# Performance work log

Measured on AMD Instinct MI355X. Metric: run time of the kernel, lower is better.

Reference implementation:

```python
import math
import jax, jax.numpy as jnp
import numpy as np

N = 8192
IN_DIM = 512
INTER = 512
HID = 1024
OUT = 512
GROUPS = 16
EPS = 1e-5


def setup_inputs() -> dict:
    key = jax.random.key(0)
    ks = jax.random.split(key, 12)
    w = lambda k, shape: jax.random.normal(k, shape, jnp.float32) * 0.02
    return {
        "h": jax.random.normal(ks[0], (N, IN_DIM), jnp.float32),
        "D": jax.random.uniform(ks[1], (N, N), dtype=jnp.float32),
        "h_prime": jax.random.normal(ks[2], (N, OUT), jnp.float32),
        "Wq": w(ks[3], (INTER, IN_DIM)), "bq": jnp.zeros((INTER,), jnp.float32),
        "Wk": w(ks[4], (INTER, IN_DIM)), "bk": jnp.zeros((INTER,), jnp.float32),
        "Wv": w(ks[5], (INTER, IN_DIM)), "bv": jnp.zeros((INTER,), jnp.float32),
        "Wr": w(ks[6], (HID, INTER)), "br": jnp.zeros((HID,), jnp.float32),
        "Wc": w(ks[7], (HID, OUT)), "bc": jnp.zeros((HID,), jnp.float32),
        "Wp": w(ks[8], (OUT, 2 * HID)), "bp": jnp.zeros((OUT,), jnp.float32),
        "alpha": jnp.full((OUT,), 0.25, jnp.float32),       # PReLU per-channel slope
        "gamma": jnp.ones((OUT,), jnp.float32),             # GroupNorm weight
        "beta": jnp.zeros((OUT,), jnp.float32),             # GroupNorm bias
    }


def reference(h, D, h_prime, Wq, bq, Wk, bk, Wv, bv, Wr, br, Wc, bc, Wp, bp, alpha, gamma, beta):
    Q = h @ Wq.T + bq                                    # [N, inter]
    K = h @ Wk.T + bk
    V = h @ Wv.T + bv
    scores = (Q @ K.T) / math.sqrt(INTER)                # [N, N]
    attn = jax.nn.softmax(D * scores, axis=-1)           # decay-masked softmax
    h_ret = attn @ V                                     # [N, inter]
    h_ret = jax.nn.gelu(h_ret @ Wr.T + br, approximate=False)  # torch GELU (erf)
    h_cat = h_prime @ Wc.T + bc                          # [N, hid]
    x = jnp.concatenate([h_ret, h_cat], axis=-1) @ Wp.T + bp   # [N, out]
    x = jnp.where(x >= 0, x, alpha * x)                  # PReLU, per-channel
    # GroupNorm over [1, out, N]: stats per group over (channels_in_group, N)
    xT = x.T                                             # [out, N]
    grp = xT.reshape(GROUPS, (OUT // GROUPS) * N)
    mean = grp.mean(axis=1, keepdims=True)
    var = grp.var(axis=1, keepdims=True)
    grp = (grp - mean) * jax.lax.rsqrt(var + EPS)
    xT = grp.reshape(OUT, N) * gamma[:, None] + beta[:, None]
    return xT.T                                          # [N, out]
```

## Files before the change

### kernel.cpp

```cpp
#include <hip/hip_runtime.h>
#include <stdint.h>
#include <math.h>

typedef float f32x4 __attribute__((ext_vector_type(4)));
typedef __bf16 bf16x8 __attribute__((ext_vector_type(8)));
typedef unsigned short u16;

#define DEVINL static __device__ __forceinline__

DEVINL u16 f2bf(float f) {
  union { float f; unsigned u; } x; x.f = f;
  unsigned r = x.u + 0x7fffu + ((x.u >> 16) & 1u);
  return (u16)(r >> 16);
}

DEVINL void gload_lds16(const void* g, void* l) {
  __builtin_amdgcn_global_load_lds(
      (__attribute__((address_space(1))) void*)(g),
      (__attribute__((address_space(3))) void*)(l), 16, 0, 0);
}

__global__ void cast_kernel(const float* __restrict__ src, u16* __restrict__ dst, int n) {
  int i = (blockIdx.x * 256 + threadIdx.x) * 4;
  if (i >= n) return;
  float4 v = *(const float4*)(src + i);
  u16 o[4] = { f2bf(v.x), f2bf(v.y), f2bf(v.z), f2bf(v.w) };
  *(uint64_t*)(dst + i) = *(uint64_t*)o;
}

template<int EPI>
__global__ __launch_bounds__(256, 2) void gemm_nt(
    const u16* __restrict__ A, int lda, const u16* __restrict__ B, int ldb,
    void* __restrict__ C, int ldc, int coff,
    const float* __restrict__ bias, const float* __restrict__ alpha,
    int N128, int K, float scale)
{
  __shared__ __align__(16) u16 at[2][128 * 64];
  __shared__ __align__(16) u16 bt[2][128 * 64];
  const int tid = threadIdx.x;
  const int w = tid >> 6, lane = tid & 63, r = lane & 15, kg = lane >> 4;
  const int bm = blockIdx.x / N128, bn = blockIdx.x % N128;
  const int m0 = bm * 128, n0 = bn * 128;

  f32x4 acc[4][4];
  #pragma unroll
  for (int m = 0; m < 4; ++m)
    #pragma unroll
    for (int n = 0; n < 4; ++n) acc[m][n] = f32x4{0.f, 0.f, 0.f, 0.f};

  const int srow = tid >> 3, sc = tid & 7;
  const int nk = K >> 6;

  #pragma unroll
  for (int i = 0; i < 4; ++i) {
    int row = srow + i * 32, cs = (sc ^ row) & 7;
    gload_lds16(A + (size_t)(m0 + row) * lda + cs * 8, at[0] + i * 2048 + w * 512);
    gload_lds16(B + (size_t)(n0 + row) * ldb + cs * 8, bt[0] + i * 2048 + w * 512);
  }
  __syncthreads();

  for (int kt = 0; kt < nk; ++kt) {
    const int cur = kt & 1;
    if (kt + 1 < nk) {
      #pragma unroll
      for (int i = 0; i < 4; ++i) {
        int row = srow + i * 32, cs = (sc ^ row) & 7;
        int kcol = (kt + 1) * 64 + cs * 8;
        gload_lds16(A + (size_t)(m0 + row) * lda + kcol, at[cur ^ 1] + i * 2048 + w * 512);
        gload_lds16(B + (size_t)(n0 + row) * ldb + kcol, bt[cur ^ 1] + i * 2048 + w * 512);
      }
    }
    #pragma unroll
    for (int ks = 0; ks < 2; ++ks) {
      bf16x8 af[4], bff[4];
      #pragma unroll
      for (int m = 0; m < 4; ++m) {
        int row = (w >> 1) * 64 + m * 16 + r;
        int cs = ((ks * 4 + kg) ^ row) & 7;
        af[m] = *(const bf16x8*)(at[cur] + row * 64 + cs * 8);
      }
      #pragma unroll
      for (int n = 0; n < 4; ++n) {
        int row = (w & 1) * 64 + n * 16 + r;
        int cs = ((ks * 4 + kg) ^ row) & 7;
        bff[n] = *(const bf16x8*)(bt[cur] + row * 64 + cs * 8);
      }
      #pragma unroll
      for (int m = 0; m < 4; ++m)
        #pragma unroll
        for (int n = 0; n < 4; ++n)
          acc[m][n] = __builtin_amdgcn_mfma_f32_16x16x32_bf16(af[m], bff[n], acc[m][n], 0, 0, 0);
    }
    __syncthreads();
  }

  #pragma unroll
  for (int m = 0; m < 4; ++m) {
    #pragma unroll
    for (int n = 0; n < 4; ++n) {
      const int gcol = n0 + (w & 1) * 64 + n * 16 + r;
      #pragma unroll
      for (int reg = 0; reg < 4; ++reg) {
        const int grow = m0 + (w >> 1) * 64 + m * 16 + kg * 4 + reg;
        float v = acc[m][n][reg];
        if (EPI == 1) v += bias[grow]; else v += bias[gcol];
        if (EPI == 0) v *= scale;
        if (EPI == 2) v = 0.5f * v * (1.f + erff(v * 0.70710678118654752f));
        if (EPI == 3) {
          float a = alpha[gcol];
          v = (v >= 0.f) ? v : a * v;
          ((float*)C)[(size_t)grow * ldc + coff + gcol] = v;
        } else {
          ((u16*)C)[(size_t)grow * ldc + coff + gcol] = f2bf(v);
        }
      }
    }
  }
}

__global__ __launch_bounds__(256, 2) void flash_kernel(
    const u16* __restrict__ Qb, const u16* __restrict__ Kb,
    const u16* __restrict__ VTb, const float* __restrict__ Dm,
    float* __restrict__ Op, float* __restrict__ lp)
{
  __shared__ __align__(16) u16 kbuf[2][64 * 128];
  __shared__ __align__(16) u16 vbuf[2][128 * 64];
  __shared__ __align__(16) u16 pbuf[4][16 * 64];
  const int tid = threadIdx.x;
  const int w = tid >> 6, lane = tid & 63, r = lane & 15, kg = lane >> 4;
  const int s = blockIdx.x & 3, qb = blockIdx.x >> 2;
  const int q0 = qb * 64;
  const int kvb = s * 2048;

  auto stage_k = [&](int buf, int kv0, int kc) {
    #pragma unroll
    for (int i = 0; i < 4; ++i) {
      const int row = (tid >> 4) + i * 16, c = tid & 15;
      const int cs = (c & 8) | ((c ^ row) & 7);
      gload_lds16(Kb + (size_t)(kv0 + row) * 512 + kc * 128 + cs * 8,
                  kbuf[buf] + i * 2048 + w * 512);
    }
  };
  auto stage_v = [&](int buf, int kv0, int dc) {
    #pragma unroll
    for (int i = 0; i < 4; ++i) {
      const int row = (tid >> 3) + i * 32, c = tid & 7;
      const int cs = (c ^ row) & 7;
      gload_lds16(VTb + (size_t)(dc * 128 + row) * 8192 + kv0 + cs * 8,
                  vbuf[buf] + i * 2048 + w * 512);
    }
  };

  bf16x8 aq[16];
  {
    const u16* qrow = Qb + (size_t)(q0 + w * 16 + r) * 512;
    #pragma unroll
    for (int ks = 0; ks < 16; ++ks) aq[ks] = *(const bf16x8*)(qrow + ks * 32 + kg * 8);
  }

  f32x4 o[32];
  #pragma unroll
  for (int i = 0; i < 32; ++i) o[i] = f32x4{0.f, 0.f, 0.f, 0.f};
  float lsum[4] = {0.f, 0.f, 0.f, 0.f};

  stage_k(0, kvb, 0);
  __syncthreads();

  #pragma unroll 1
  for (int j = 0; j < 32; ++j) {
    const int kv0 = kvb + j * 64;
    f32x4 sacc[4];
    #pragma unroll
    for (int t = 0; t < 4; ++t) sacc[t] = f32x4{0.f, 0.f, 0.f, 0.f};
    float dv[4][4];

    #pragma unroll
    for (int kc = 0; kc < 4; ++kc) {
      if (kc < 3) stage_k((kc + 1) & 1, kv0, kc + 1);
      else        stage_v(0, kv0, 0);
      if (kc == 1) {
        const float* db = Dm + (size_t)(q0 + w * 16 + kg * 4) * 8192 + kv0 + r;
        #pragma unroll
        for (int t = 0; t < 4; ++t)
          #pragma unroll
          for (int reg = 0; reg < 4; ++reg)
            dv[t][reg] = __builtin_nontemporal_load(db + (size_t)reg * 8192 + t * 16);
      }
      #pragma unroll
      for (int ks2 = 0; ks2 < 4; ++ks2) {
        const bf16x8 a = aq[kc * 4 + ks2];
        #pragma unroll
        for (int t = 0; t < 4; ++t) {
          const int row = t * 16 + r;
          const int c = ks2 * 4 + kg;
          const int cs = (c & 8) | ((c ^ row) & 7);
          const bf16x8 b = *(const bf16x8*)(kbuf[kc & 1] + row * 128 + cs * 8);
          sacc[t] = __builtin_amdgcn_mfma_f32_16x16x32_bf16(a, b, sacc[t], 0, 0, 0);
        }
      }
      if (kc == 3) {
        #pragma unroll
        for (int t = 0; t < 4; ++t) {
          #pragma unroll
          for (int reg = 0; reg < 4; ++reg) {
            const float pv = __expf(sacc[t][reg] * dv[t][reg]);
            lsum[reg] += pv;
            const int prow = kg * 4 + reg, pcol = t * 16 + r;
            const int byt = prow * 128 + (((pcol >> 3) ^ prow) & 7) * 16 + (pcol & 7) * 2;
            *(u16*)((char*)pbuf[w] + byt) = f2bf(pv);
          }
        }
      }
      __syncthreads();
    }

    bf16x8 ap[2];
    #pragma unroll
    for (int ks = 0; ks < 2; ++ks) {
      const int cs = ((ks * 4 + kg) ^ r) & 7;
      ap[ks] = *(const bf16x8*)((const char*)pbuf[w] + r * 128 + cs * 16);
    }

    #pragma unroll
    for (int dc = 0; dc < 4; ++dc) {
      if (dc < 3)        stage_v((dc + 1) & 1, kv0, dc + 1);
      else if (j < 31)   stage_k(0, kv0 + 64, 0);
      #pragma unroll
      for (int t2 = 0; t2 < 8; ++t2) {
        const int row = t2 * 16 + r;
        #pragma unroll
        for (int ks = 0; ks < 2; ++ks) {
          const int cs = ((ks * 4 + kg) ^ row) & 7;
          const bf16x8 b = *(const bf16x8*)(vbuf[dc & 1] + row * 64 + cs * 8);
          o[dc * 8 + t2] = __builtin_amdgcn_mfma_f32_16x16x32_bf16(ap[ks], b, o[dc * 8 + t2], 0, 0, 0);
        }
      }
      __syncthreads();
    }
  }

  #pragma unroll
  for (int reg = 0; reg < 4; ++reg) {
    float v = lsum[reg];
    v += __shfl_xor(v, 1); v += __shfl_xor(v, 2);
    v += __shfl_xor(v, 4); v += __shfl_xor(v, 8);
    lsum[reg] = v;
  }

  float* ob = Op + (size_t)s * (8192 * 512) + (size_t)(q0 + w * 16 + kg * 4) * 512 + r;
  #pragma unroll
  for (int ti = 0; ti < 32; ++ti)
    #pragma unroll
    for (int reg = 0; reg < 4; ++reg)
      ob[(size_t)reg * 512 + ti * 16] = o[ti][reg];

  if (r == 0) {
    #pragma unroll
    for (int reg = 0; reg < 4; ++reg)
      lp[(size_t)s * 8192 + q0 + w * 16 + kg * 4 + reg] = lsum[reg];
  }
}

__global__ void combine_kernel(const float* __restrict__ Op, const float* __restrict__ lp,
                               u16* __restrict__ hrb) {
  const int idx = (blockIdx.x * 256 + threadIdx.x) * 4;
  const int q = idx >> 9;
  const float li = 1.f / (lp[q] + lp[8192 + q] + lp[16384 + q] + lp[24576 + q]);
  float4 a = *(const float4*)(Op + idx);
  const float4 b = *(const float4*)(Op + 4194304 + idx);
  const float4 c = *(const float4*)(Op + 8388608 + idx);
  const float4 d = *(const float4*)(Op + 12582912 + idx);
  a.x += b.x + c.x + d.x; a.y += b.y + c.y + d.y;
  a.z += b.z + c.z + d.z; a.w += b.w + c.w + d.w;
  u16 o[4] = { f2bf(a.x * li), f2bf(a.y * li), f2bf(a.z * li), f2bf(a.w * li) };
  *(uint64_t*)(hrb + idx) = *(uint64_t*)o;
}

__global__ void gn_stats_kernel(const float* __restrict__ x, float* __restrict__ part) {
  const int g = blockIdx.x >> 4, ch = blockIdx.x & 15;
  const int t = threadIdx.x;
  float s = 0.f, ss = 0.f;
  const int cl = (t & 7) * 4;
  const int r0 = ch * 512 + (t >> 3);
  for (int i = 0; i < 16; ++i) {
    const float4 v = *(const float4*)(x + (size_t)(r0 + i * 32) * 512 + g * 32 + cl);
    s += v.x + v.y + v.z + v.w;
    ss += v.x * v.x + v.y * v.y + v.z * v.z + v.w * v.w;
  }
  #pragma unroll
  for (int m = 1; m < 64; m <<= 1) { s += __shfl_xor(s, m); ss += __shfl_xor(ss, m); }
  __shared__ float red[8];
  const int w = t >> 6, lane = t & 63;
  if (lane == 0) { red[w * 2] = s; red[w * 2 + 1] = ss; }
  __syncthreads();
  if (t == 0) {
    part[blockIdx.x * 2]     = red[0] + red[2] + red[4] + red[6];
    part[blockIdx.x * 2 + 1] = red[1] + red[3] + red[5] + red[7];
  }
}

__global__ void gn_finalize_kernel(const float* __restrict__ part, float* __restrict__ mv) {
  const int g = threadIdx.x;
  if (g < 16) {
    float s = 0.f, ss = 0.f;
    for (int ch = 0; ch < 16; ++ch) {
      s  += part[(g * 16 + ch) * 2];
      ss += part[(g * 16 + ch) * 2 + 1];
    }
    const float mean = s * (1.f / 262144.f);
    const float var = ss * (1.f / 262144.f) - mean * mean;
    mv[g * 2] = mean;
    mv[g * 2 + 1] = rsqrtf(var + 1e-5f);
  }
}

__global__ void gn_norm_kernel(const float* __restrict__ x, const float* __restrict__ mv,
                               const float* __restrict__ gamma, const float* __restrict__ beta,
                               float* __restrict__ out) {
  const int idx = (blockIdx.x * 256 + threadIdx.x) * 4;
  const int c = idx & 511, g = c >> 5;
  const float mean = mv[g * 2], rs = mv[g * 2 + 1];
  float4 v = *(const float4*)(x + idx);
  const float4 gm = *(const float4*)(gamma + c);
  const float4 bt = *(const float4*)(beta + c);
  v.x = (v.x - mean) * rs * gm.x + bt.x;
  v.y = (v.y - mean) * rs * gm.y + bt.y;
  v.z = (v.z - mean) * rs * gm.z + bt.z;
  v.w = (v.w - mean) * rs * gm.w + bt.w;
  *(float4*)(out + idx) = v;
}

extern "C" void kernel_launch(void* const* d_in, const int* in_sizes, int n_in,
                              void* d_out, int out_size, void* d_ws, size_t ws_size,
                              hipStream_t stream) {
  (void)in_sizes; (void)n_in; (void)out_size; (void)ws_size;
  const float* h     = (const float*)d_in[0];
  const float* Dm    = (const float*)d_in[1];
  const float* hp    = (const float*)d_in[2];
  const float* Wq    = (const float*)d_in[3];
  const float* bq    = (const float*)d_in[4];
  const float* Wk    = (const float*)d_in[5];
  const float* bk    = (const float*)d_in[6];
  const float* Wv    = (const float*)d_in[7];
  const float* bv    = (const float*)d_in[8];
  const float* Wr    = (const float*)d_in[9];
  const float* br    = (const float*)d_in[10];
  const float* Wc    = (const float*)d_in[11];
  const float* bc    = (const float*)d_in[12];
  const float* Wp    = (const float*)d_in[13];
  const float* bp    = (const float*)d_in[14];
  const float* alpha = (const float*)d_in[15];
  const float* gamma = (const float*)d_in[16];
  const float* beta  = (const float*)d_in[17];

  char* ws = (char*)d_ws;
  u16*   hb   = (u16*)(ws + 0);
  u16*   hpb  = (u16*)(ws + 8388608);
  u16*   Qb   = (u16*)(ws + 16777216);
  u16*   Kb   = (u16*)(ws + 25165824);
  u16*   VTb  = (u16*)(ws + 33554432);
  u16*   hrb  = (u16*)(ws + 41943040);
  u16*   Wqb  = (u16*)(ws + 50331648);
  u16*   Wkb  = (u16*)(ws + 50855936);
  u16*   Wvb  = (u16*)(ws + 51380224);
  u16*   Wrb  = (u16*)(ws + 51904512);
  u16*   Wcb  = (u16*)(ws + 52953088);
  u16*   Wpb  = (u16*)(ws + 54001664);
  u16*   xcat = (u16*)(ws + 56098816);
  float* xf   = (float*)(ws + 89653248);
  float* Op   = (float*)(ws + 106430464);
  float* lp   = (float*)(ws + 173539328);
  float* gp   = (float*)(ws + 173670400);
  float* mv   = (float*)(ws + 173672448);

  cast_kernel<<<4096, 256, 0, stream>>>(h, hb, 4194304);
  cast_kernel<<<4096, 256, 0, stream>>>(hp, hpb, 4194304);
  cast_kernel<<<256, 256, 0, stream>>>(Wq, Wqb, 262144);
  cast_kernel<<<256, 256, 0, stream>>>(Wk, Wkb, 262144);
  cast_kernel<<<256, 256, 0, stream>>>(Wv, Wvb, 262144);
  cast_kernel<<<512, 256, 0, stream>>>(Wr, Wrb, 524288);
  cast_kernel<<<512, 256, 0, stream>>>(Wc, Wcb, 524288);
  cast_kernel<<<1024, 256, 0, stream>>>(Wp, Wpb, 1048576);

  gemm_nt<0><<<256, 256, 0, stream>>>(hb, 512, Wqb, 512, Qb, 512, 0, bq, nullptr, 4, 512, 0.044194173824159216f);
  gemm_nt<0><<<256, 256, 0, stream>>>(hb, 512, Wkb, 512, Kb, 512, 0, bk, nullptr, 4, 512, 1.0f);
  gemm_nt<1><<<256, 256, 0, stream>>>(Wvb, 512, hb, 512, VTb, 8192, 0, bv, nullptr, 64, 512, 1.0f);

  flash_kernel<<<512, 256, 0, stream>>>(Qb, Kb, VTb, Dm, Op, lp);
  combine_kernel<<<4096, 256, 0, stream>>>(Op, lp, hrb);

  gemm_nt<2><<<512, 256, 0, stream>>>(hrb, 512, Wrb, 512, xcat, 2048, 0, br, nullptr, 8, 512, 1.0f);
  gemm_nt<0><<<512, 256, 0, stream>>>(hpb, 512, Wcb, 512, xcat, 2048, 1024, bc, nullptr, 8, 512, 1.0f);
  gemm_nt<3><<<256, 256, 0, stream>>>(xcat, 2048, Wpb, 2048, xf, 512, 0, bp, alpha, 4, 2048, 1.0f);

  gn_stats_kernel<<<256, 256, 0, stream>>>(xf, gp);
  gn_finalize_kernel<<<1, 64, 0, stream>>>(gp, mv);
  gn_norm_kernel<<<4096, 256, 0, stream>>>(xf, mv, gamma, beta, (float*)d_out);
}
```

Before: 504.1 us.

## Replace K/V double buffers with a 4-slot LDS ring prefetched three stages ahead

The flash kernel's separate K and V double buffers become a single 4-slot LDS ring fed by a 9-phase schedule per KV tile: 4 K chunks, 1 D tile, then 4 V chunks. Loads are issued three phases ahead and gated by s_waitcnt vmcnt plus one barrier per phase, instead of the old synchronous refill pattern. The decay matrix D is now staged through LDS with async global-to-LDS loads rather than read directly into registers, and the MFMA sections are wrapped in s_setprio raises. This aims to hide global memory latency better and reduce barrier stalls, at the cost of more complex ring indexing and a redundant prefetch on the last iteration.

```diff
diff --git a/kernel.cpp b/kernel.cpp
--- a/kernel.cpp
+++ b/kernel.cpp
@@ -123,8 +123,7 @@
     const u16* __restrict__ VTb, const float* __restrict__ Dm,
     float* __restrict__ Op, float* __restrict__ lp)
 {
-  __shared__ __align__(16) u16 kbuf[2][64 * 128];
-  __shared__ __align__(16) u16 vbuf[2][128 * 64];
+  __shared__ __align__(16) u16 ring[4][8192];
   __shared__ __align__(16) u16 pbuf[4][16 * 64];
   const int tid = threadIdx.x;
   const int w = tid >> 6, lane = tid & 63, r = lane & 15, kg = lane >> 4;
@@ -132,22 +131,37 @@
   const int q0 = qb * 64;
   const int kvb = s * 2048;
 
-  auto stage_k = [&](int buf, int kv0, int kc) {
+  const int rK = tid >> 4, cK = tid & 15;
+  const int rV = tid >> 3, cV = tid & 7;
+
+  auto issueK = [&](int jj, int kc, int buf) {
+    const u16* src = Kb + (size_t)(kvb + jj * 64) * 512 + kc * 128;
+    u16* dst = ring[buf];
     #pragma unroll
     for (int i = 0; i < 4; ++i) {
-      const int row = (tid >> 4) + i * 16, c = tid & 15;
-      const int cs = (c & 8) | ((c ^ row) & 7);
-      gload_lds16(Kb + (size_t)(kv0 + row) * 512 + kc * 128 + cs * 8,
-                  kbuf[buf] + i * 2048 + w * 512);
+      const int row = rK + i * 16;
+      const int cs = (cK & 8) | ((cK ^ row) & 7);
+      gload_lds16(src + (size_t)row * 512 + cs * 8, dst + i * 2048 + w * 512);
     }
   };
-  auto stage_v = [&](int buf, int kv0, int dc) {
+  auto issueD = [&](int jj, int buf) {
+    const float* src = Dm + (size_t)q0 * 8192 + kvb + jj * 64;
+    u16* dst = ring[buf];
     #pragma unroll
     for (int i = 0; i < 4; ++i) {
-      const int row = (tid >> 3) + i * 32, c = tid & 7;
-      const int cs = (c ^ row) & 7;
-      gload_lds16(VTb + (size_t)(dc * 128 + row) * 8192 + kv0 + cs * 8,
-                  vbuf[buf] + i * 2048 + w * 512);
+      const int row = rK + i * 16;
+      const int g = cK ^ (row & 15);
+      gload_lds16(src + (size_t)row * 8192 + g * 4, dst + i * 2048 + w * 512);
+    }
+  };
+  auto issueV = [&](int jj, int dc, int buf) {
+    const u16* src = VTb + (size_t)(dc * 128) * 8192 + kvb + jj * 64;
+    u16* dst = ring[buf];
+    #pragma unroll
+    for (int i = 0; i < 4; ++i) {
+      const int row = rV + i * 32;
+      const int cs = (cV ^ row) & 7;
+      gload_lds16(src + (size_t)row * 8192 + cs * 8, dst + i * 2048 + w * 512);
     }
   };
 
@@ -163,79 +177,91 @@
   for (int i = 0; i < 32; ++i) o[i] = f32x4{0.f, 0.f, 0.f, 0.f};
   float lsum[4] = {0.f, 0.f, 0.f, 0.f};
 
-  stage_k(0, kvb, 0);
-  __syncthreads();
+  issueK(0, 0, 0);
+  issueK(0, 1, 1);
+  issueK(0, 2, 2);
 
   #pragma unroll 1
   for (int j = 0; j < 32; ++j) {
-    const int kv0 = kvb + j * 64;
     f32x4 sacc[4];
     #pragma unroll
     for (int t = 0; t < 4; ++t) sacc[t] = f32x4{0.f, 0.f, 0.f, 0.f};
-    float dv[4][4];
-
-    #pragma unroll
-    for (int kc = 0; kc < 4; ++kc) {
-      if (kc < 3) stage_k((kc + 1) & 1, kv0, kc + 1);
-      else        stage_v(0, kv0, 0);
-      if (kc == 1) {
-        const float* db = Dm + (size_t)(q0 + w * 16 + kg * 4) * 8192 + kv0 + r;
-        #pragma unroll
-        for (int t = 0; t < 4; ++t)
+    bf16x8 ap[2];
+
+    #pragma unroll
+    for (int p = 0; p < 9; ++p) {
+      asm volatile("s_waitcnt vmcnt(8)" ::: "memory");
+      __builtin_amdgcn_s_barrier();
+      {
+        int pp = p + 3, jj = j;
+        if (pp >= 9) { pp -= 9; jj = (j < 31) ? j + 1 : 31; }
+        const int buf = (j + p + 3) & 3;
+        if (pp < 4)       issueK(jj, pp, buf);
+        else if (pp == 4) issueD(jj, buf);
+        else              issueV(jj, pp - 5, buf);
+      }
+      const int cbuf = (j + p) & 3;
+
+      if (p < 4) {
+        const u16* cb = ring[cbuf];
+        __builtin_amdgcn_s_setprio(1);
+        #pragma unroll
+        for (int ks2 = 0; ks2 < 4; ++ks2) {
+          const bf16x8 a = aq[p * 4 + ks2];
           #pragma unroll
-          for (int reg = 0; reg < 4; ++reg)
-            dv[t][reg] = __builtin_nontemporal_load(db + (size_t)reg * 8192 + t * 16);
-      }
-      #pragma unroll
-      for (int ks2 = 0; ks2 < 4; ++ks2) {
-        const bf16x8 a = aq[kc * 4 + ks2];
-        #pragma unroll
-        for (int t = 0; t < 4; ++t) {
-          const int row = t * 16 + r;
-          const int c = ks2 * 4 + kg;
-          const int cs = (c & 8) | ((c ^ row) & 7);
-          const bf16x8 b = *(const bf16x8*)(kbuf[kc & 1] + row * 128 + cs * 8);
-          sacc[t] = __builtin_amdgcn_mfma_f32_16x16x32_bf16(a, b, sacc[t], 0, 0, 0);
-        }
-      }
-      if (kc == 3) {
+          for (int t = 0; t < 4; ++t) {
+            const int row = t * 16 + r;
+            const int c = ks2 * 4 + kg;
+            const int cs = (c & 8) | ((c ^ row) & 7);
+            const bf16x8 b = *(const bf16x8*)(cb + row * 128 + cs * 8);
+            sacc[t] = __builtin_amdgcn_mfma_f32_16x16x32_bf16(a, b, sacc[t], 0, 0, 0);
+          }
+        }
+        __builtin_amdgcn_s_setprio(0);
+      } else if (p == 4) {
+        const char* db = (const char*)ring[cbuf];
+        float dvv[16];
+        #pragma unroll
+        for (int reg = 0; reg < 4; ++reg) {
+          const int row = w * 16 + kg * 4 + reg;
+          #pragma unroll
+          for (int t = 0; t < 4; ++t) {
+            const int slot = (t * 4 + (r >> 2)) ^ (row & 15);
+            dvv[t * 4 + reg] = *(const float*)(db + row * 256 + slot * 16 + (r & 3) * 4);
+          }
+        }
         #pragma unroll
         for (int t = 0; t < 4; ++t) {
           #pragma unroll
           for (int reg = 0; reg < 4; ++reg) {
-            const float pv = __expf(sacc[t][reg] * dv[t][reg]);
+            const float pv = __expf(sacc[t][reg] * dvv[t * 4 + reg]);
             lsum[reg] += pv;
             const int prow = kg * 4 + reg, pcol = t * 16 + r;
             const int byt = prow * 128 + (((pcol >> 3) ^ prow) & 7) * 16 + (pcol & 7) * 2;
             *(u16*)((char*)pbuf[w] + byt) = f2bf(pv);
           }
         }
-      }
-      __syncthreads();
-    }
-
-    bf16x8 ap[2];
-    #pragma unroll
-    for (int ks = 0; ks < 2; ++ks) {
-      const int cs = ((ks * 4 + kg) ^ r) & 7;
-      ap[ks] = *(const bf16x8*)((const char*)pbuf[w] + r * 128 + cs * 16);
-    }
-
-    #pragma unroll
-    for (int dc = 0; dc < 4; ++dc) {
-      if (dc < 3)        stage_v((dc + 1) & 1, kv0, dc + 1);
-      else if (j < 31)   stage_k(0, kv0 + 64, 0);
-      #pragma unroll
-      for (int t2 = 0; t2 < 8; ++t2) {
-        const int row = t2 * 16 + r;
         #pragma unroll
         for (int ks = 0; ks < 2; ++ks) {
-          const int cs = ((ks * 4 + kg) ^ row) & 7;
-          const bf16x8 b = *(const bf16x8*)(vbuf[dc & 1] + row * 64 + cs * 8);
-          o[dc * 8 + t2] = __builtin_amdgcn_mfma_f32_16x16x32_bf16(ap[ks], b, o[dc * 8 + t2], 0, 0, 0);
-        }
-      }
-      __syncthreads();
+          const int cs = ((ks * 4 + kg) ^ r) & 7;
+          ap[ks] = *(const bf16x8*)((const char*)pbuf[w] + r * 128 + cs * 16);
+        }
+      } else {
+        const int dc = p - 5;
+        const u16* vb = ring[cbuf];
+        __builtin_amdgcn_s_setprio(1);
+        #pragma unroll
+        for (int t2 = 0; t2 < 8; ++t2) {
+          const int row = t2 * 16 + r;
+          #pragma unroll
+          for (int ks = 0; ks < 2; ++ks) {
+            const int cs = ((ks * 4 + kg) ^ row) & 7;
+            const bf16x8 b = *(const bf16x8*)(vb + row * 64 + cs * 8);
+            o[dc * 8 + t2] = __builtin_amdgcn_mfma_f32_16x16x32_bf16(ap[ks], b, o[dc * 8 + t2], 0, 0, 0);
+          }
+        }
+        __builtin_amdgcn_s_setprio(0);
+      }
     }
   }
 
```

New measurement: 607.3 us. +20.5%, slower.

## Replace fused flash attention with materialized score GEMM, exp pass, and PV GEMM

Applied to the files above, without the earlier changes.

The fused split-KV flash kernel and its combine pass are removed. Attention now runs as three steps: a QK^T GEMM writes the full 8192x8192 score matrix in bf16, an elementwise kernel applies the decay, exponentiates and takes row sums in place, and a second GEMM multiplies by V^T and divides by the row sum in its epilogue. This reuses the tuned GEMM and drops the per-split partial output buffers, but adds a 128MB bf16 score round trip through memory. It also adds XCD-aware block remapping for the large GEMMs and reuses workspace regions between stages.

```diff
diff --git a/kernel.cpp b/kernel.cpp
--- a/kernel.cpp
+++ b/kernel.cpp
@@ -4,6 +4,7 @@
 
 typedef float f32x4 __attribute__((ext_vector_type(4)));
 typedef __bf16 bf16x8 __attribute__((ext_vector_type(8)));
+typedef unsigned int u32x4 __attribute__((ext_vector_type(4)));
 typedef unsigned short u16;
 
 #define DEVINL static __device__ __forceinline__
@@ -33,13 +34,16 @@
     const u16* __restrict__ A, int lda, const u16* __restrict__ B, int ldb,
     void* __restrict__ C, int ldc, int coff,
     const float* __restrict__ bias, const float* __restrict__ alpha,
-    int N128, int K, float scale)
+    int N128, int K, float scale, int map)
 {
   __shared__ __align__(16) u16 at[2][128 * 64];
   __shared__ __align__(16) u16 bt[2][128 * 64];
   const int tid = threadIdx.x;
   const int w = tid >> 6, lane = tid & 63, r = lane & 15, kg = lane >> 4;
-  const int bm = blockIdx.x / N128, bn = blockIdx.x % N128;
+  int bm, bn;
+  if (map == 1)      { const int x = blockIdx.x & 7, i = blockIdx.x >> 3; bm = x * 8 + (i >> 2); bn = i & 3; }
+  else if (map == 2) { const int x = blockIdx.x & 7, i = blockIdx.x >> 3; bm = x * 8 + (i >> 6); bn = i & 63; }
+  else               { bm = blockIdx.x / N128; bn = blockIdx.x % N128; }
   const int m0 = bm * 128, n0 = bn * 128;
 
   f32x4 acc[4][4];
@@ -103,10 +107,13 @@
       for (int reg = 0; reg < 4; ++reg) {
         const int grow = m0 + (w >> 1) * 64 + m * 16 + kg * 4 + reg;
         float v = acc[m][n][reg];
-        if (EPI == 1) v += bias[grow]; else v += bias[gcol];
-        if (EPI == 0) v *= scale;
-        if (EPI == 2) v = 0.5f * v * (1.f + erff(v * 0.70710678118654752f));
+        if (EPI == 0) v = (v + bias[gcol]) * scale;
+        if (EPI == 1) v = v + bias[grow];
+        if (EPI == 2) { v += bias[gcol]; v = 0.5f * v * (1.f + erff(v * 0.70710678118654752f)); }
+        if (EPI == 4) v = v * scale;
+        if (EPI == 5) v = v / bias[grow];
         if (EPI == 3) {
+          v += bias[gcol];
           float a = alpha[gcol];
           v = (v >= 0.f) ? v : a * v;
           ((float*)C)[(size_t)grow * ldc + coff + gcol] = v;
@@ -118,162 +125,38 @@
   }
 }
 
-__global__ __launch_bounds__(256, 2) void flash_kernel(
-    const u16* __restrict__ Qb, const u16* __restrict__ Kb,
-    const u16* __restrict__ VTb, const float* __restrict__ Dm,
-    float* __restrict__ Op, float* __restrict__ lp)
+__global__ __launch_bounds__(256) void exp_kernel(
+    u16* __restrict__ SP, const float* __restrict__ Dm, float* __restrict__ ls)
 {
-  __shared__ __align__(16) u16 kbuf[2][64 * 128];
-  __shared__ __align__(16) u16 vbuf[2][128 * 64];
-  __shared__ __align__(16) u16 pbuf[4][16 * 64];
-  const int tid = threadIdx.x;
-  const int w = tid >> 6, lane = tid & 63, r = lane & 15, kg = lane >> 4;
-  const int s = blockIdx.x & 3, qb = blockIdx.x >> 2;
-  const int q0 = qb * 64;
-  const int kvb = s * 2048;
-
-  auto stage_k = [&](int buf, int kv0, int kc) {
-    #pragma unroll
-    for (int i = 0; i < 4; ++i) {
-      const int row = (tid >> 4) + i * 16, c = tid & 15;
-      const int cs = (c & 8) | ((c ^ row) & 7);
-      gload_lds16(Kb + (size_t)(kv0 + row) * 512 + kc * 128 + cs * 8,
-                  kbuf[buf] + i * 2048 + w * 512);
-    }
-  };
-  auto stage_v = [&](int buf, int kv0, int dc) {
-    #pragma unroll
-    for (int i = 0; i < 4; ++i) {
-      const int row = (tid >> 3) + i * 32, c = tid & 7;
-      const int cs = (c ^ row) & 7;
-      gload_lds16(VTb + (size_t)(dc * 128 + row) * 8192 + kv0 + cs * 8,
-                  vbuf[buf] + i * 2048 + w * 512);
-    }
-  };
-
-  bf16x8 aq[16];
-  {
-    const u16* qrow = Qb + (size_t)(q0 + w * 16 + r) * 512;
-    #pragma unroll
-    for (int ks = 0; ks < 16; ++ks) aq[ks] = *(const bf16x8*)(qrow + ks * 32 + kg * 8);
-  }
-
-  f32x4 o[32];
-  #pragma unroll
-  for (int i = 0; i < 32; ++i) o[i] = f32x4{0.f, 0.f, 0.f, 0.f};
-  float lsum[4] = {0.f, 0.f, 0.f, 0.f};
-
-  stage_k(0, kvb, 0);
-  __syncthreads();
-
-  #pragma unroll 1
-  for (int j = 0; j < 32; ++j) {
-    const int kv0 = kvb + j * 64;
-    f32x4 sacc[4];
-    #pragma unroll
-    for (int t = 0; t < 4; ++t) sacc[t] = f32x4{0.f, 0.f, 0.f, 0.f};
-    float dv[4][4];
-
-    #pragma unroll
-    for (int kc = 0; kc < 4; ++kc) {
-      if (kc < 3) stage_k((kc + 1) & 1, kv0, kc + 1);
-      else        stage_v(0, kv0, 0);
-      if (kc == 1) {
-        const float* db = Dm + (size_t)(q0 + w * 16 + kg * 4) * 8192 + kv0 + r;
-        #pragma unroll
-        for (int t = 0; t < 4; ++t)
-          #pragma unroll
-          for (int reg = 0; reg < 4; ++reg)
-            dv[t][reg] = __builtin_nontemporal_load(db + (size_t)reg * 8192 + t * 16);
-      }
-      #pragma unroll
-      for (int ks2 = 0; ks2 < 4; ++ks2) {
-        const bf16x8 a = aq[kc * 4 + ks2];
-        #pragma unroll
-        for (int t = 0; t < 4; ++t) {
-          const int row = t * 16 + r;
-          const int c = ks2 * 4 + kg;
-          const int cs = (c & 8) | ((c ^ row) & 7);
-          const bf16x8 b = *(const bf16x8*)(kbuf[kc & 1] + row * 128 + cs * 8);
-          sacc[t] = __builtin_amdgcn_mfma_f32_16x16x32_bf16(a, b, sacc[t], 0, 0, 0);
-        }
-      }
-      if (kc == 3) {
-        #pragma unroll
-        for (int t = 0; t < 4; ++t) {
-          #pragma unroll
-          for (int reg = 0; reg < 4; ++reg) {
-            const float pv = __expf(sacc[t][reg] * dv[t][reg]);
-            lsum[reg] += pv;
-            const int prow = kg * 4 + reg, pcol = t * 16 + r;
-            const int byt = prow * 128 + (((pcol >> 3) ^ prow) & 7) * 16 + (pcol & 7) * 2;
-            *(u16*)((char*)pbuf[w] + byt) = f2bf(pv);
-          }
-        }
-      }
-      __syncthreads();
-    }
-
-    bf16x8 ap[2];
-    #pragma unroll
-    for (int ks = 0; ks < 2; ++ks) {
-      const int cs = ((ks * 4 + kg) ^ r) & 7;
-      ap[ks] = *(const bf16x8*)((const char*)pbuf[w] + r * 128 + cs * 16);
-    }
-
-    #pragma unroll
-    for (int dc = 0; dc < 4; ++dc) {
-      if (dc < 3)        stage_v((dc + 1) & 1, kv0, dc + 1);
-      else if (j < 31)   stage_k(0, kv0 + 64, 0);
-      #pragma unroll
-      for (int t2 = 0; t2 < 8; ++t2) {
-        const int row = t2 * 16 + r;
-        #pragma unroll
-        for (int ks = 0; ks < 2; ++ks) {
-          const int cs = ((ks * 4 + kg) ^ row) & 7;
-          const bf16x8 b = *(const bf16x8*)(vbuf[dc & 1] + row * 64 + cs * 8);
-          o[dc * 8 + t2] = __builtin_amdgcn_mfma_f32_16x16x32_bf16(ap[ks], b, o[dc * 8 + t2], 0, 0, 0);
-        }
-      }
-      __syncthreads();
-    }
-  }
-
-  #pragma unroll
-  for (int reg = 0; reg < 4; ++reg) {
-    float v = lsum[reg];
-    v += __shfl_xor(v, 1); v += __shfl_xor(v, 2);
-    v += __shfl_xor(v, 4); v += __shfl_xor(v, 8);
-    lsum[reg] = v;
-  }
-
-  float* ob = Op + (size_t)s * (8192 * 512) + (size_t)(q0 + w * 16 + kg * 4) * 512 + r;
-  #pragma unroll
-  for (int ti = 0; ti < 32; ++ti)
-    #pragma unroll
-    for (int reg = 0; reg < 4; ++reg)
-      ob[(size_t)reg * 512 + ti * 16] = o[ti][reg];
-
-  if (r == 0) {
-    #pragma unroll
-    for (int reg = 0; reg < 4; ++reg)
-      lp[(size_t)s * 8192 + q0 + w * 16 + kg * 4 + reg] = lsum[reg];
-  }
-}
-
-__global__ void combine_kernel(const float* __restrict__ Op, const float* __restrict__ lp,
-                               u16* __restrict__ hrb) {
-  const int idx = (blockIdx.x * 256 + threadIdx.x) * 4;
-  const int q = idx >> 9;
-  const float li = 1.f / (lp[q] + lp[8192 + q] + lp[16384 + q] + lp[24576 + q]);
-  float4 a = *(const float4*)(Op + idx);
-  const float4 b = *(const float4*)(Op + 4194304 + idx);
-  const float4 c = *(const float4*)(Op + 8388608 + idx);
-  const float4 d = *(const float4*)(Op + 12582912 + idx);
-  a.x += b.x + c.x + d.x; a.y += b.y + c.y + d.y;
-  a.z += b.z + c.z + d.z; a.w += b.w + c.w + d.w;
-  u16 o[4] = { f2bf(a.x * li), f2bf(a.y * li), f2bf(a.z * li), f2bf(a.w * li) };
-  *(uint64_t*)(hrb + idx) = *(uint64_t*)o;
+  const int w = threadIdx.x >> 6, lane = threadIdx.x & 63;
+  const int row = blockIdx.x * 4 + w;
+  u16* sp = SP + (size_t)row * 8192;
+  const float* dp = Dm + (size_t)row * 8192;
+  float acc = 0.f;
+  #pragma unroll 2
+  for (int it = 0; it < 16; ++it) {
+    const int c = it * 512 + lane * 8;
+    const u32x4 sv = *(const u32x4*)(sp + c);
+    const u32x4 d0 = __builtin_nontemporal_load((const u32x4*)(dp + c));
+    const u32x4 d1 = __builtin_nontemporal_load((const u32x4*)(dp + c + 4));
+    u32x4 ow;
+    #pragma unroll
+    for (int kp = 0; kp < 4; ++kp) {
+      union { unsigned u; float f; } s0, s1, e0, e1;
+      s0.u = (sv[kp] & 0xffffu) << 16;
+      s1.u = sv[kp] & 0xffff0000u;
+      e0.u = (kp < 2) ? d0[kp * 2] : d1[(kp - 2) * 2];
+      e1.u = (kp < 2) ? d0[kp * 2 + 1] : d1[(kp - 2) * 2 + 1];
+      const float p0 = __expf(s0.f * e0.f);
+      const float p1 = __expf(s1.f * e1.f);
+      acc += p0 + p1;
+      ow[kp] = (unsigned)f2bf(p0) | ((unsigned)f2bf(p1) << 16);
+    }
+    *(u32x4*)(sp + c) = ow;
+  }
+  #pragma unroll
+  for (int m = 1; m < 64; m <<= 1) acc += __shfl_xor(acc, m);
+  if (lane == 0) ls[row] = acc;
 }
 
 __global__ void gn_stats_kernel(const float* __restrict__ x, float* __restrict__ part) {
@@ -354,24 +237,25 @@
   const float* beta  = (const float*)d_in[17];
 
   char* ws = (char*)d_ws;
-  u16*   hb   = (u16*)(ws + 0);
-  u16*   hpb  = (u16*)(ws + 8388608);
-  u16*   Qb   = (u16*)(ws + 16777216);
-  u16*   Kb   = (u16*)(ws + 25165824);
-  u16*   VTb  = (u16*)(ws + 33554432);
-  u16*   hrb  = (u16*)(ws + 41943040);
-  u16*   Wqb  = (u16*)(ws + 50331648);
-  u16*   Wkb  = (u16*)(ws + 50855936);
-  u16*   Wvb  = (u16*)(ws + 51380224);
-  u16*   Wrb  = (u16*)(ws + 51904512);
-  u16*   Wcb  = (u16*)(ws + 52953088);
-  u16*   Wpb  = (u16*)(ws + 54001664);
-  u16*   xcat = (u16*)(ws + 56098816);
-  float* xf   = (float*)(ws + 89653248);
-  float* Op   = (float*)(ws + 106430464);
-  float* lp   = (float*)(ws + 173539328);
-  float* gp   = (float*)(ws + 173670400);
-  float* mv   = (float*)(ws + 173672448);
+  const size_t MB = 1ull << 20;
+  u16*   S    = (u16*)(ws);
+  u16*   hb   = (u16*)(ws);
+  u16*   xcat = (u16*)(ws);
+  float* xf   = (float*)(ws + 32 * MB);
+  u16*   hpb  = (u16*)(ws + 128 * MB);
+  u16*   Qb   = (u16*)(ws + 144 * MB);
+  u16*   hrb  = (u16*)(ws + 144 * MB);
+  u16*   Kb   = (u16*)(ws + 152 * MB);
+  u16*   VTb  = (u16*)(ws + 160 * MB);
+  u16*   Wqb  = (u16*)(ws + 168 * MB);
+  u16*   Wkb  = Wqb + 262144;
+  u16*   Wvb  = Wkb + 262144;
+  u16*   Wrb  = Wvb + 262144;
+  u16*   Wcb  = Wrb + 524288;
+  u16*   Wpb  = Wcb + 524288;
+  float* lsum = (float*)(ws + 168 * MB + 5767168);
+  float* gp   = lsum + 8192;
+  float* mv   = gp + 512;
 
   cast_kernel<<<4096, 256, 0, stream>>>(h, hb, 4194304);
   cast_kernel<<<4096, 256, 0, stream>>>(hp, hpb, 4194304);
@@ -382,16 +266,20 @@
   cast_kernel<<<512, 256, 0, stream>>>(Wc, Wcb, 524288);
   cast_kernel<<<1024, 256, 0, stream>>>(Wp, Wpb, 1048576);
 
-  gemm_nt<0><<<256, 256, 0, stream>>>(hb, 512, Wqb, 512, Qb, 512, 0, bq, nullptr, 4, 512, 0.044194173824159216f);
-  gemm_nt<0><<<256, 256, 0, stream>>>(hb, 512, Wkb, 512, Kb, 512, 0, bk, nullptr, 4, 512, 1.0f);
-  gemm_nt<1><<<256, 256, 0, stream>>>(Wvb, 512, hb, 512, VTb, 8192, 0, bv, nullptr, 64, 512, 1.0f);
-
-  flash_kernel<<<512, 256, 0, stream>>>(Qb, Kb, VTb, Dm, Op, lp);
-  combine_kernel<<<4096, 256, 0, stream>>>(Op, lp, hrb);
-
-  gemm_nt<2><<<512, 256, 0, stream>>>(hrb, 512, Wrb, 512, xcat, 2048, 0, br, nullptr, 8, 512, 1.0f);
-  gemm_nt<0><<<512, 256, 0, stream>>>(hpb, 512, Wcb, 512, xcat, 2048, 1024, bc, nullptr, 8, 512, 1.0f);
-  gemm_nt<3><<<256, 256, 0, stream>>>(xcat, 2048, Wpb, 2048, xf, 512, 0, bp, alpha, 4, 2048, 1.0f);
+  gemm_nt<0><<<256, 256, 0, stream>>>(hb, 512, Wqb, 512, Qb, 512, 0, bq, nullptr, 4, 512, 0.044194173824159216f, 0);
+  gemm_nt<0><<<256, 256, 0, stream>>>(hb, 512, Wkb, 512, Kb, 512, 0, bk, nullptr, 4, 512, 1.0f, 0);
+  gemm_nt<1><<<256, 256, 0, stream>>>(Wvb, 512, hb, 512, VTb, 8192, 0, bv, nullptr, 64, 512, 1.0f, 0);
+
+  gemm_nt<4><<<4096, 256, 0, stream>>>(Qb, 512, Kb, 512, S, 8192, 0, nullptr, nullptr, 64, 512, 1.0f, 2);
+
+  exp_kernel<<<2048, 256, 0, stream>>>(S, Dm, lsum);
+
+  gemm_nt<5><<<256, 256, 0, stream>>>(S, 8192, VTb, 8192, hrb, 512, 0, lsum, nullptr, 4, 8192, 1.0f, 1);
+
+  gemm_nt<2><<<512, 256, 0, stream>>>(hrb, 512, Wrb, 512, xcat, 2048, 0, br, nullptr, 8, 512, 1.0f, 0);
+  gemm_nt<0><<<512, 256, 0, stream>>>(hpb, 512, Wcb, 512, xcat, 2048, 1024, bc, nullptr, 8, 512, 1.0f, 0);
+
+  gemm_nt<3><<<256, 256, 0, stream>>>(xcat, 2048, Wpb, 2048, xf, 512, 0, bp, alpha, 4, 2048, 1.0f, 0);
 
   gn_stats_kernel<<<256, 256, 0, stream>>>(xf, gp);
   gn_finalize_kernel<<<1, 64, 0, stream>>>(gp, mv);
```

Result: faster. 462.8 us (-8.2%).
